# Kernel tuning notes

Hardware: AMD Instinct MI355X
Metric: run time of the kernel (lower is better)

## Reference

```python
import jax, jax.numpy as jnp
import numpy as np
from jax import lax

DIM = 2048
K = 3


def rms_norm(x):
    eps = jnp.asarray(jnp.finfo(x.dtype).eps, x.dtype)
    var = jnp.mean(jnp.square(x), axis=-1, keepdims=True)
    return x * lax.rsqrt(var + eps)


def causal_dwconv1d(y, w, b, dilation):
    # y: [B, S, D]; w: [D, 1, K]; depthwise causal conv along S
    yc = jnp.transpose(y, (0, 2, 1))  # [B, D, S]
    pad = (K - 1) * dilation
    out = lax.conv_general_dilated(
        yc, w.astype(yc.dtype),
        window_strides=(1,),
        padding=[(pad, 0)],
        rhs_dilation=(dilation,),
        dimension_numbers=('NCH', 'OIH', 'NCH'),
        feature_group_count=DIM,
    )
    out = out + b.astype(yc.dtype)[None, :, None]
    return jnp.transpose(out, (0, 2, 1))  # [B, S, D]


def setup_inputs() -> dict:
    key = jax.random.key(0)
    ks = jax.random.split(key, 4)
    B, S, D = 4, 4096, DIM
    x = jax.random.normal(ks[0], (B, S, D), dtype=jnp.float32)
    W_expand = jax.random.normal(ks[1], (3 * D, D), dtype=jnp.float32) * (1.0 / np.sqrt(D))
    conv_w = jax.random.normal(ks[2], (D, 1, K), dtype=jnp.float32) * (1.0 / K)
    conv_b = jnp.zeros((D,), dtype=jnp.float32)
    W_proj = jax.random.normal(ks[3], (D, D), dtype=jnp.float32) * (1.0 / np.sqrt(D))
    conv_scale = jnp.ones((D,), dtype=jnp.float32)
    return {"x": x, "W_expand": W_expand, "conv_w": conv_w, "conv_b": conv_b,
            "W_proj": W_proj, "conv_scale": conv_scale, "dilation": 1}


def reference(x, W_expand, conv_w, conv_b, W_proj, conv_scale, dilation):
    h = jnp.einsum('bsd,ed->bse', rms_norm(x), W_expand.astype(x.dtype))
    B_gate, C_gate, z = jnp.split(h, 3, axis=-1)
    y = B_gate * z  # squared_gate=False
    y = causal_dwconv1d(y, conv_w, conv_b, dilation)
    o = C_gate * y
    o = jnp.einsum('bsd,ed->bse', o, W_proj.astype(x.dtype))
    return x + conv_scale.astype(x.dtype)[None, None, :] * o
```

## Files before the change

kernel.cpp:

```cpp
#include <hip/hip_runtime.h>
#include <hip/hip_bf16.h>
#include <stdint.h>

typedef __bf16 bf16;
typedef __bf16 bf16x8 __attribute__((ext_vector_type(8)));
typedef __bf16 bf16x4 __attribute__((ext_vector_type(4)));
typedef float  floatx4 __attribute__((ext_vector_type(4)));

#define DIMD 2048
#define BATB 4
#define SEQS 4096
#define MTOT (BATB*SEQS)

#define BAR()    __builtin_amdgcn_s_barrier()
#define LGKMC(N) asm volatile("s_waitcnt lgkmcnt(" #N ")" ::: "memory")
#define VMC6()   asm volatile("s_waitcnt vmcnt(6)" ::: "memory")
#define VMC0()   asm volatile("s_waitcnt vmcnt(0)" ::: "memory")
#define SCHED0() __builtin_amdgcn_sched_barrier(0)

__device__ __forceinline__ void gload_lds16(const bf16* g, bf16* l) {
    __builtin_amdgcn_global_load_lds(
        (const __attribute__((address_space(1))) void*)g,
        (__attribute__((address_space(3))) void*)l,
        16, 0, 0);
}

__global__ __launch_bounds__(256) void f2bf_k(const float* __restrict__ src,
                                              bf16* __restrict__ dst, int n) {
    int i = (blockIdx.x * 256 + threadIdx.x) * 4;
    if (i >= n) return;
    float4 v = *(const float4*)&src[i];
    bf16x4 o;
    o[0] = (bf16)v.x; o[1] = (bf16)v.y; o[2] = (bf16)v.z; o[3] = (bf16)v.w;
    *(bf16x4*)&dst[i] = o;
}

__global__ __launch_bounds__(256) void rmsnorm_k(const float* __restrict__ x,
                                                 bf16* __restrict__ xn) {
    const int row = blockIdx.x;
    const int tid = threadIdx.x;
    const float* xr = x + (size_t)row * DIMD;
    float4 a = *(const float4*)&xr[tid * 8];
    float4 b = *(const float4*)&xr[tid * 8 + 4];
    float s = a.x*a.x + a.y*a.y + a.z*a.z + a.w*a.w
            + b.x*b.x + b.y*b.y + b.z*b.z + b.w*b.w;
    #pragma unroll
    for (int off = 32; off > 0; off >>= 1) s += __shfl_down(s, off);
    __shared__ float red[4];
    if ((tid & 63) == 0) red[tid >> 6] = s;
    __syncthreads();
    float tot = red[0] + red[1] + red[2] + red[3];
    float sc = rsqrtf(tot * (1.0f / DIMD) + 1.1920929e-07f);
    bf16x8 o;
    o[0] = (bf16)(a.x * sc); o[1] = (bf16)(a.y * sc);
    o[2] = (bf16)(a.z * sc); o[3] = (bf16)(a.w * sc);
    o[4] = (bf16)(b.x * sc); o[5] = (bf16)(b.y * sc);
    o[6] = (bf16)(b.z * sc); o[7] = (bf16)(b.w * sc);
    *(bf16x8*)&xn[(size_t)row * DIMD + tid * 8] = o;
}

__global__ __launch_bounds__(256) void gateconv_k(const bf16* __restrict__ h,
                                                  const float* __restrict__ cw,
                                                  const float* __restrict__ cb,
                                                  bf16* __restrict__ o,
                                                  const int* __restrict__ dil_p) {
    int gid = blockIdx.x * 256 + threadIdx.x;
    int m = gid >> 9;
    int d = (gid & 511) << 2;
    int s = m & (SEQS - 1);
    int dil = dil_p[0];
    const bf16* hr = h + (size_t)m * (3 * DIMD);

    bf16x4 Cv = *(const bf16x4*)&hr[DIMD + d];
    bf16x4 B0 = *(const bf16x4*)&hr[d];
    bf16x4 Z0 = *(const bf16x4*)&hr[2 * DIMD + d];
    float y0[4], y1[4], y2[4];
    #pragma unroll
    for (int j = 0; j < 4; ++j) y0[j] = (float)B0[j] * (float)Z0[j];
    if (s >= dil) {
        const bf16* h1 = hr - (size_t)dil * 3 * DIMD;
        bf16x4 B1 = *(const bf16x4*)&h1[d];
        bf16x4 Z1 = *(const bf16x4*)&h1[2 * DIMD + d];
        #pragma unroll
        for (int j = 0; j < 4; ++j) y1[j] = (float)B1[j] * (float)Z1[j];
    } else {
        #pragma unroll
        for (int j = 0; j < 4; ++j) y1[j] = 0.0f;
    }
    if (s >= 2 * dil) {
        const bf16* h2 = hr - (size_t)(2 * dil) * 3 * DIMD;
        bf16x4 B2 = *(const bf16x4*)&h2[d];
        bf16x4 Z2 = *(const bf16x4*)&h2[2 * DIMD + d];
        #pragma unroll
        for (int j = 0; j < 4; ++j) y2[j] = (float)B2[j] * (float)Z2[j];
    } else {
        #pragma unroll
        for (int j = 0; j < 4; ++j) y2[j] = 0.0f;
    }
    bf16x4 ov;
    #pragma unroll
    for (int j = 0; j < 4; ++j) {
        float w0 = cw[(d + j) * 3 + 0];
        float w1 = cw[(d + j) * 3 + 1];
        float w2 = cw[(d + j) * 3 + 2];
        float conv = w0 * y2[j] + w1 * y1[j] + w2 * y0[j] + cb[d + j];
        ov[j] = (bf16)((float)Cv[j] * conv);
    }
    *(bf16x4*)&o[(size_t)m * DIMD + d] = ov;
}

template<int RESID>
__global__ __launch_bounds__(512, 2) void gemm_bt(const bf16* __restrict__ A,
                                                  const bf16* __restrict__ B,
                                                  bf16* __restrict__ Hout,
                                                  float* __restrict__ Fout,
                                                  const float* __restrict__ resid,
                                                  const float* __restrict__ scale,
                                                  int M, int N, int K) {
    __shared__ __align__(16) bf16 smem[2][32768];
    const int tid = threadIdx.x;
    const int wave = tid >> 6;
    const int lane = tid & 63;
    const int quad = lane >> 4;
    const int col16 = lane & 15;

    const int nx   = (int)gridDim.x;
    const int nwg  = nx * (int)gridDim.y;
    const int orig = (int)blockIdx.y * nx + (int)blockIdx.x;
    const int lin  = (orig & 7) * (nwg >> 3) + (orig >> 3);
    const int n0 = (lin % nx) * 256;
    const int m0 = (lin / nx) * 256;

    const int wm = (wave >> 2) * 128;
    const int wn = (wave & 3) * 64;

    const int srow = tid >> 3;
    const int cs   = (tid & 7) ^ (srow & 7);
    const bf16* aSrc = A + (size_t)(m0 + srow) * K + cs * 8;
    const bf16* bSrc = B + (size_t)(n0 + srow) * K + cs * 8;
    const int stbase = wave * 512;
    const size_t K64  = (size_t)K * 64;
    const size_t K128 = (size_t)K * 128;

    const int rsw = col16 & 7;
    const int ard = (wm + col16) * 64;
    const int brd = (wn + col16) * 64;
    const int sl0 = ((0 + quad) ^ rsw) * 8;
    const int sl1 = ((4 + quad) ^ rsw) * 8;

    bf16x8 Bf[4][2];
    bf16x8 A0[2][2], A1[2][2], A2[2][2], A3[2][2];
    floatx4 acc[4][2][4];
    #pragma unroll
    for (int q = 0; q < 4; ++q)
        #pragma unroll
        for (int f = 0; f < 2; ++f)
            #pragma unroll
            for (int n = 0; n < 4; ++n) acc[q][f][n] = (floatx4)0.0f;

    auto stage = [&](const bf16* src, bf16* dstBase, int t, int h) {
        const bf16* s = src + (size_t)h * K128 + (size_t)t * 64;
        bf16* d = dstBase + h * 8192 + stbase;
        gload_lds16(s, d);
        gload_lds16(s + K64, d + 4096);
    };
    auto ldA = [&](bf16x8 (&q)[2][2], const bf16* Asb, int f0) {
        #pragma unroll
        for (int f = 0; f < 2; ++f) {
            const bf16* p = Asb + ard + (f0 + f) * (16 * 64);
            q[f][0] = *(const bf16x8*)(p + sl0);
            q[f][1] = *(const bf16x8*)(p + sl1);
        }
    };
    auto ldB = [&](const bf16* Bsb) {
        #pragma unroll
        for (int n = 0; n < 4; ++n) {
            const bf16* p = Bsb + brd + n * (16 * 64);
            Bf[n][0] = *(const bf16x8*)(p + sl0);
            Bf[n][1] = *(const bf16x8*)(p + sl1);
        }
    };
    auto mm = [&](floatx4 (&ac)[2][4], bf16x8 (&a)[2][2]) {
        __builtin_amdgcn_s_setprio(1);
        #pragma unroll
        for (int f = 0; f < 2; ++f)
            #pragma unroll
            for (int n = 0; n < 4; ++n) {
                ac[f][n] = __builtin_amdgcn_mfma_f32_16x16x32_bf16(a[f][0], Bf[n][0], ac[f][n], 0, 0, 0);
                ac[f][n] = __builtin_amdgcn_mfma_f32_16x16x32_bf16(a[f][1], Bf[n][1], ac[f][n], 0, 0, 0);
            }
        __builtin_amdgcn_s_setprio(0);
    };

    const int NT = K >> 6;

    stage(aSrc, smem[0],         0, 0);
    stage(aSrc, smem[0],         0, 1);
    stage(bSrc, smem[0] + 16384, 0, 0);
    stage(bSrc, smem[0] + 16384, 0, 1);
    stage(bSrc, smem[1] + 16384, 1, 0);
    stage(bSrc, smem[1] + 16384, 1, 1);
    stage(aSrc, smem[1],         1, 0);
    VMC6();
    BAR();
    ldB(smem[0] + 16384);
    ldA(A0, smem[0], 0);
    SCHED0();

    for (int t = 0; t < NT - 2; ++t) {
        const int b = t & 1;
        const bf16* Acur = smem[b];
        bf16* Awr = smem[b];
        bf16* Bwr = smem[b] + 16384;
        bf16* Aoth = smem[b ^ 1];
        const bf16* Anxt = smem[b ^ 1];
        const bf16* Bnxt = smem[b ^ 1] + 16384;
        ldA(A1, Acur, 2);
        stage(aSrc, Aoth, t + 1, 1);
        SCHED0(); BAR(); LGKMC(4); SCHED0();
        mm(acc[0], A0);
        BAR();
        ldA(A2, Acur, 4);
        stage(bSrc, Bwr, t + 2, 0);
        SCHED0(); BAR(); LGKMC(4); SCHED0();
        mm(acc[1], A1);
        BAR();
        ldA(A3, Acur, 6);
        stage(bSrc, Bwr, t + 2, 1);
        SCHED0(); BAR(); LGKMC(4); SCHED0();
        mm(acc[2], A2);
        BAR();
        stage(aSrc, Awr, t + 2, 0);
        VMC6();
        BAR(); LGKMC(0); SCHED0();
        mm(acc[3], A3);
        SCHED0();
        ldB(Bnxt);
        ldA(A0, Anxt, 0);
        SCHED0(); BAR();
    }
    {
        const int t = NT - 2;
        const int b = t & 1;
        const bf16* Acur = smem[b];
        bf16* Aoth = smem[b ^ 1];
        const bf16* Anxt = smem[b ^ 1];
        const bf16* Bnxt = smem[b ^ 1] + 16384;
        ldA(A1, Acur, 2);
        stage(aSrc, Aoth, t + 1, 1);
        SCHED0(); BAR(); LGKMC(4); SCHED0();
        mm(acc[0], A0);
        BAR();
        ldA(A2, Acur, 4);
        SCHED0(); BAR(); LGKMC(4); SCHED0();
        mm(acc[1], A1);
        BAR();
        ldA(A3, Acur, 6);
        SCHED0(); BAR(); LGKMC(4); SCHED0();
        mm(acc[2], A2);
        BAR();
        VMC0();
        BAR(); LGKMC(0); SCHED0();
        mm(acc[3], A3);
        SCHED0();
        ldB(Bnxt);
        ldA(A0, Anxt, 0);
        SCHED0(); BAR();
    }
    {
        const int b = (NT - 1) & 1;
        const bf16* Acur = smem[b];
        ldA(A1, Acur, 2);
        SCHED0(); BAR(); LGKMC(4); SCHED0();
        mm(acc[0], A0);
        BAR();
        ldA(A2, Acur, 4);
        SCHED0(); BAR(); LGKMC(4); SCHED0();
        mm(acc[1], A1);
        BAR();
        ldA(A3, Acur, 6);
        SCHED0(); BAR(); LGKMC(4); SCHED0();
        mm(acc[2], A2);
        BAR();
        LGKMC(0); SCHED0();
        mm(acc[3], A3);
    }

    #pragma unroll
    for (int q2 = 0; q2 < 4; ++q2)
        #pragma unroll
        for (int f = 0; f < 2; ++f)
            #pragma unroll
            for (int n = 0; n < 4; ++n) {
                const int c  = n0 + wn + n * 16 + col16;
                const int rb = m0 + wm + (q2 * 2 + f) * 16 + quad * 4;
                #pragma unroll
                for (int r = 0; r < 4; ++r) {
                    size_t off = (size_t)(rb + r) * N + c;
                    float v = acc[q2][f][n][r];
                    if (RESID) {
                        Fout[off] = resid[off] + scale[c] * v;
                    } else {
                        Hout[off] = (bf16)v;
                    }
                }
            }
}

extern "C" void kernel_launch(void* const* d_in, const int* in_sizes, int n_in,
                              void* d_out, int out_size, void* d_ws, size_t ws_size,
                              hipStream_t stream) {
    const float* x  = (const float*)d_in[0];
    const float* We = (const float*)d_in[1];
    const float* cw = (const float*)d_in[2];
    const float* cb = (const float*)d_in[3];
    const float* Wp = (const float*)d_in[4];
    const float* cs = (const float*)d_in[5];
    const int*   dil = (const int*)d_in[6];

    char* ws = (char*)d_ws;
    bf16* xn  = (bf16*)ws;
    bf16* Web = (bf16*)(ws + 67108864);
    bf16* Wpb = (bf16*)(ws + 67108864 + 25165824);
    bf16* h   = (bf16*)(ws + 100663296);

    f2bf_k<<<(3 * DIMD * DIMD / 4 + 255) / 256, 256, 0, stream>>>(We, Web, 3 * DIMD * DIMD);
    f2bf_k<<<(DIMD * DIMD / 4 + 255) / 256, 256, 0, stream>>>(Wp, Wpb, DIMD * DIMD);
    rmsnorm_k<<<MTOT, 256, 0, stream>>>(x, xn);
    gemm_bt<0><<<dim3(3 * DIMD / 256, MTOT / 256), 512, 0, stream>>>(
        xn, Web, h, nullptr, nullptr, nullptr, MTOT, 3 * DIMD, DIMD);
    gateconv_k<<<(MTOT * (DIMD / 4)) / 256, 256, 0, stream>>>(h, cw, cb, xn , dil);
    gemm_bt<1><<<dim3(DIMD / 256, MTOT / 256), 512, 0, stream>>>(
        xn , Wpb, nullptr, (float*)d_out, x, cs, MTOT, DIMD, DIMD);
}
```

Before: 836.9 us.

## Switch GEMM to 32x32x16 MFMA with coarser K-phase pipeline and nontemporal stores

```diff
diff --git a/kernel.cpp b/kernel.cpp
--- a/kernel.cpp
+++ b/kernel.cpp
@@ -5,7 +5,7 @@
 typedef __bf16 bf16;
 typedef __bf16 bf16x8 __attribute__((ext_vector_type(8)));
 typedef __bf16 bf16x4 __attribute__((ext_vector_type(4)));
-typedef float  floatx4 __attribute__((ext_vector_type(4)));
+typedef float  floatx16 __attribute__((ext_vector_type(16)));
 
 #define DIMD 2048
 #define BATB 4
@@ -14,7 +14,7 @@
 
 #define BAR()    __builtin_amdgcn_s_barrier()
 #define LGKMC(N) asm volatile("s_waitcnt lgkmcnt(" #N ")" ::: "memory")
-#define VMC6()   asm volatile("s_waitcnt vmcnt(6)" ::: "memory")
+#define VMC4()   asm volatile("s_waitcnt vmcnt(4)" ::: "memory")
 #define VMC0()   asm volatile("s_waitcnt vmcnt(0)" ::: "memory")
 #define SCHED0() __builtin_amdgcn_sched_barrier(0)
 
@@ -71,7 +71,7 @@
     int dil = dil_p[0];
     const bf16* hr = h + (size_t)m * (3 * DIMD);
 
-    bf16x4 Cv = *(const bf16x4*)&hr[DIMD + d];
+    bf16x4 Cv = __builtin_nontemporal_load((const bf16x4*)&hr[DIMD + d]);
     bf16x4 B0 = *(const bf16x4*)&hr[d];
     bf16x4 Z0 = *(const bf16x4*)&hr[2 * DIMD + d];
     float y0[4], y1[4], y2[4];
@@ -121,8 +121,9 @@
     const int tid = threadIdx.x;
     const int wave = tid >> 6;
     const int lane = tid & 63;
-    const int quad = lane >> 4;
-    const int col16 = lane & 15;
+    const int l31 = lane & 31;
+    const int hi = lane >> 5;
+    const int l7 = lane & 7;
 
     const int nx   = (int)gridDim.x;
     const int nwg  = nx * (int)gridDim.y;
@@ -142,21 +143,18 @@
     const size_t K64  = (size_t)K * 64;
     const size_t K128 = (size_t)K * 128;
 
-    const int rsw = col16 & 7;
-    const int ard = (wm + col16) * 64;
-    const int brd = (wn + col16) * 64;
-    const int sl0 = ((0 + quad) ^ rsw) * 8;
-    const int sl1 = ((4 + quad) ^ rsw) * 8;
-
-    bf16x8 Bf[4][2];
-    bf16x8 A0[2][2], A1[2][2], A2[2][2], A3[2][2];
-    floatx4 acc[4][2][4];
-    #pragma unroll
-    for (int q = 0; q < 4; ++q)
-        #pragma unroll
-        for (int f = 0; f < 2; ++f)
-            #pragma unroll
-            for (int n = 0; n < 4; ++n) acc[q][f][n] = (floatx4)0.0f;
+    const int arow = (wm + l31) * 64;
+    const int brow = (wn + l31) * 64;
+    const int slotk[4] = { ((0 + hi) ^ l7) * 8, ((2 + hi) ^ l7) * 8,
+                           ((4 + hi) ^ l7) * 8, ((6 + hi) ^ l7) * 8 };
+
+    bf16x8 Afr[4][4];
+    bf16x8 Bfr[4][2];
+    floatx16 acc[4][2];
+    #pragma unroll
+    for (int mi = 0; mi < 4; ++mi)
+        #pragma unroll
+        for (int ni = 0; ni < 2; ++ni) acc[mi][ni] = (floatx16)0.0f;
 
     auto stage = [&](const bf16* src, bf16* dstBase, int t, int h) {
         const bf16* s = src + (size_t)h * K128 + (size_t)t * 64;
@@ -164,32 +162,23 @@
         gload_lds16(s, d);
         gload_lds16(s + K64, d + 4096);
     };
-    auto ldA = [&](bf16x8 (&q)[2][2], const bf16* Asb, int f0) {
-        #pragma unroll
-        for (int f = 0; f < 2; ++f) {
-            const bf16* p = Asb + ard + (f0 + f) * (16 * 64);
-            q[f][0] = *(const bf16x8*)(p + sl0);
-            q[f][1] = *(const bf16x8*)(p + sl1);
-        }
+    auto ldAk = [&](const bf16* Asb, int ks) {
+        #pragma unroll
+        for (int mi = 0; mi < 4; ++mi)
+            Afr[ks][mi] = *(const bf16x8*)(Asb + arow + mi * (32 * 64) + slotk[ks]);
     };
-    auto ldB = [&](const bf16* Bsb) {
-        #pragma unroll
-        for (int n = 0; n < 4; ++n) {
-            const bf16* p = Bsb + brd + n * (16 * 64);
-            Bf[n][0] = *(const bf16x8*)(p + sl0);
-            Bf[n][1] = *(const bf16x8*)(p + sl1);
-        }
+    auto ldBk = [&](const bf16* Bsb, int ks) {
+        #pragma unroll
+        for (int ni = 0; ni < 2; ++ni)
+            Bfr[ks][ni] = *(const bf16x8*)(Bsb + brow + ni * (32 * 64) + slotk[ks]);
     };
-    auto mm = [&](floatx4 (&ac)[2][4], bf16x8 (&a)[2][2]) {
-        __builtin_amdgcn_s_setprio(1);
-        #pragma unroll
-        for (int f = 0; f < 2; ++f)
+    auto mmk = [&](int ks) {
+        #pragma unroll
+        for (int mi = 0; mi < 4; ++mi)
             #pragma unroll
-            for (int n = 0; n < 4; ++n) {
-                ac[f][n] = __builtin_amdgcn_mfma_f32_16x16x32_bf16(a[f][0], Bf[n][0], ac[f][n], 0, 0, 0);
-                ac[f][n] = __builtin_amdgcn_mfma_f32_16x16x32_bf16(a[f][1], Bf[n][1], ac[f][n], 0, 0, 0);
-            }
-        __builtin_amdgcn_s_setprio(0);
+            for (int ni = 0; ni < 2; ++ni)
+                acc[mi][ni] = __builtin_amdgcn_mfma_f32_32x32x16_bf16(
+                    Afr[ks][mi], Bfr[ks][ni], acc[mi][ni], 0, 0, 0);
     };
 
     const int NT = K >> 6;
@@ -200,43 +189,38 @@
     stage(bSrc, smem[0] + 16384, 0, 1);
     stage(bSrc, smem[1] + 16384, 1, 0);
     stage(bSrc, smem[1] + 16384, 1, 1);
-    stage(aSrc, smem[1],         1, 0);
-    VMC6();
+    VMC4();
     BAR();
-    ldB(smem[0] + 16384);
-    ldA(A0, smem[0], 0);
+    ldBk(smem[0] + 16384, 0); ldBk(smem[0] + 16384, 1);
+    ldBk(smem[0] + 16384, 2); ldBk(smem[0] + 16384, 3);
+    ldAk(smem[0], 0); ldAk(smem[0], 1);
     SCHED0();
 
     for (int t = 0; t < NT - 2; ++t) {
         const int b = t & 1;
         const bf16* Acur = smem[b];
-        bf16* Awr = smem[b];
         bf16* Bwr = smem[b] + 16384;
         bf16* Aoth = smem[b ^ 1];
         const bf16* Anxt = smem[b ^ 1];
         const bf16* Bnxt = smem[b ^ 1] + 16384;
-        ldA(A1, Acur, 2);
+        ldAk(Acur, 2); ldAk(Acur, 3);
+        stage(aSrc, Aoth, t + 1, 0);
         stage(aSrc, Aoth, t + 1, 1);
-        SCHED0(); BAR(); LGKMC(4); SCHED0();
-        mm(acc[0], A0);
+        SCHED0(); BAR(); LGKMC(8); SCHED0();
+        __builtin_amdgcn_s_setprio(1);
+        mmk(0); mmk(1);
+        __builtin_amdgcn_s_setprio(0);
         BAR();
-        ldA(A2, Acur, 4);
         stage(bSrc, Bwr, t + 2, 0);
-        SCHED0(); BAR(); LGKMC(4); SCHED0();
-        mm(acc[1], A1);
-        BAR();
-        ldA(A3, Acur, 6);
         stage(bSrc, Bwr, t + 2, 1);
-        SCHED0(); BAR(); LGKMC(4); SCHED0();
-        mm(acc[2], A2);
-        BAR();
-        stage(aSrc, Awr, t + 2, 0);
-        VMC6();
+        VMC4();
         BAR(); LGKMC(0); SCHED0();
-        mm(acc[3], A3);
+        __builtin_amdgcn_s_setprio(1);
+        mmk(2); mmk(3);
+        __builtin_amdgcn_s_setprio(0);
         SCHED0();
-        ldB(Bnxt);
-        ldA(A0, Anxt, 0);
+        ldBk(Bnxt, 0); ldBk(Bnxt, 1); ldBk(Bnxt, 2); ldBk(Bnxt, 3);
+        ldAk(Anxt, 0); ldAk(Anxt, 1);
         SCHED0(); BAR();
     }
     {
@@ -246,65 +230,57 @@
         bf16* Aoth = smem[b ^ 1];
         const bf16* Anxt = smem[b ^ 1];
         const bf16* Bnxt = smem[b ^ 1] + 16384;
-        ldA(A1, Acur, 2);
+        ldAk(Acur, 2); ldAk(Acur, 3);
+        stage(aSrc, Aoth, t + 1, 0);
         stage(aSrc, Aoth, t + 1, 1);
-        SCHED0(); BAR(); LGKMC(4); SCHED0();
-        mm(acc[0], A0);
-        BAR();
-        ldA(A2, Acur, 4);
-        SCHED0(); BAR(); LGKMC(4); SCHED0();
-        mm(acc[1], A1);
-        BAR();
-        ldA(A3, Acur, 6);
-        SCHED0(); BAR(); LGKMC(4); SCHED0();
-        mm(acc[2], A2);
+        SCHED0(); BAR(); LGKMC(8); SCHED0();
+        __builtin_amdgcn_s_setprio(1);
+        mmk(0); mmk(1);
+        __builtin_amdgcn_s_setprio(0);
         BAR();
         VMC0();
         BAR(); LGKMC(0); SCHED0();
-        mm(acc[3], A3);
+        __builtin_amdgcn_s_setprio(1);
+        mmk(2); mmk(3);
+        __builtin_amdgcn_s_setprio(0);
         SCHED0();
-        ldB(Bnxt);
-        ldA(A0, Anxt, 0);
+        ldBk(Bnxt, 0); ldBk(Bnxt, 1); ldBk(Bnxt, 2); ldBk(Bnxt, 3);
+        ldAk(Anxt, 0); ldAk(Anxt, 1);
         SCHED0(); BAR();
     }
     {
         const int b = (NT - 1) & 1;
         const bf16* Acur = smem[b];
-        ldA(A1, Acur, 2);
-        SCHED0(); BAR(); LGKMC(4); SCHED0();
-        mm(acc[0], A0);
-        BAR();
-        ldA(A2, Acur, 4);
-        SCHED0(); BAR(); LGKMC(4); SCHED0();
-        mm(acc[1], A1);
-        BAR();
-        ldA(A3, Acur, 6);
-        SCHED0(); BAR(); LGKMC(4); SCHED0();
-        mm(acc[2], A2);
-        BAR();
+        ldAk(Acur, 2); ldAk(Acur, 3);
+        SCHED0(); BAR(); LGKMC(8); SCHED0();
+        __builtin_amdgcn_s_setprio(1);
+        mmk(0); mmk(1);
+        __builtin_amdgcn_s_setprio(0);
         LGKMC(0); SCHED0();
-        mm(acc[3], A3);
-    }
-
-    #pragma unroll
-    for (int q2 = 0; q2 < 4; ++q2)
-        #pragma unroll
-        for (int f = 0; f < 2; ++f)
+        __builtin_amdgcn_s_setprio(1);
+        mmk(2); mmk(3);
+        __builtin_amdgcn_s_setprio(0);
+    }
+
+    #pragma unroll
+    for (int mi = 0; mi < 4; ++mi)
+        #pragma unroll
+        for (int ni = 0; ni < 2; ++ni) {
+            const int c  = n0 + wn + ni * 32 + l31;
+            const int rb = m0 + wm + mi * 32 + 4 * hi;
             #pragma unroll
-            for (int n = 0; n < 4; ++n) {
-                const int c  = n0 + wn + n * 16 + col16;
-                const int rb = m0 + wm + (q2 * 2 + f) * 16 + quad * 4;
-                #pragma unroll
-                for (int r = 0; r < 4; ++r) {
-                    size_t off = (size_t)(rb + r) * N + c;
-                    float v = acc[q2][f][n][r];
-                    if (RESID) {
-                        Fout[off] = resid[off] + scale[c] * v;
-                    } else {
-                        Hout[off] = (bf16)v;
-                    }
+            for (int reg = 0; reg < 16; ++reg) {
+                const int r = rb + (reg & 3) + 8 * (reg >> 2);
+                size_t off = (size_t)r * N + c;
+                float v = acc[mi][ni][reg];
+                if (RESID) {
+                    float rv = __builtin_nontemporal_load(&resid[off]);
+                    __builtin_nontemporal_store(rv + scale[c] * v, &Fout[off]);
+                } else {
+                    __builtin_nontemporal_store((bf16)v, &Hout[off]);
                 }
             }
+        }
 }
 
 extern "C" void kernel_launch(void* const* d_in, const int* in_sizes, int n_in,
```

Result: slower. 878.5 us (+5.0%).

## Tile gateconv over 16 sequence rows with a register sliding window

Applied to the files above, without the earlier changes.

```diff
diff --git a/kernel.cpp b/kernel.cpp
--- a/kernel.cpp
+++ b/kernel.cpp
@@ -64,49 +64,95 @@
                                                   const float* __restrict__ cb,
                                                   bf16* __restrict__ o,
                                                   const int* __restrict__ dil_p) {
-    int gid = blockIdx.x * 256 + threadIdx.x;
-    int m = gid >> 9;
-    int d = (gid & 511) << 2;
-    int s = m & (SEQS - 1);
-    int dil = dil_p[0];
-    const bf16* hr = h + (size_t)m * (3 * DIMD);
-
-    bf16x4 Cv = *(const bf16x4*)&hr[DIMD + d];
-    bf16x4 B0 = *(const bf16x4*)&hr[d];
-    bf16x4 Z0 = *(const bf16x4*)&hr[2 * DIMD + d];
-    float y0[4], y1[4], y2[4];
+    const int tid = threadIdx.x;
+    const int d = tid * 8;
+    const int m0 = blockIdx.x * 16;
+    const int s0 = m0 & (SEQS - 1);
+    const int dil = dil_p[0];
+
+    float w0[8], w1[8], w2[8], bias[8];
     #pragma unroll
-    for (int j = 0; j < 4; ++j) y0[j] = (float)B0[j] * (float)Z0[j];
-    if (s >= dil) {
-        const bf16* h1 = hr - (size_t)dil * 3 * DIMD;
-        bf16x4 B1 = *(const bf16x4*)&h1[d];
-        bf16x4 Z1 = *(const bf16x4*)&h1[2 * DIMD + d];
-        #pragma unroll
-        for (int j = 0; j < 4; ++j) y1[j] = (float)B1[j] * (float)Z1[j];
+    for (int j = 0; j < 8; ++j) {
+        w0[j]   = cw[(d + j) * 3 + 0];
+        w1[j]   = cw[(d + j) * 3 + 1];
+        w2[j]   = cw[(d + j) * 3 + 2];
+        bias[j] = cb[d + j];
+    }
+
+    if (dil == 1) {
+        float y1[8], y2[8];
+        if (s0 >= 1) {
+            const bf16* hp = h + (size_t)(m0 - 1) * (3 * DIMD);
+            bf16x8 Bv = *(const bf16x8*)&hp[d];
+            bf16x8 Zv = *(const bf16x8*)&hp[2 * DIMD + d];
+            #pragma unroll
+            for (int j = 0; j < 8; ++j) y1[j] = (float)Bv[j] * (float)Zv[j];
+            const bf16* hq = h + (size_t)(m0 - 2) * (3 * DIMD);
+            bf16x8 Bw = *(const bf16x8*)&hq[d];
+            bf16x8 Zw = *(const bf16x8*)&hq[2 * DIMD + d];
+            #pragma unroll
+            for (int j = 0; j < 8; ++j) y2[j] = (float)Bw[j] * (float)Zw[j];
+        } else {
+            #pragma unroll
+            for (int j = 0; j < 8; ++j) { y1[j] = 0.0f; y2[j] = 0.0f; }
+        }
+        for (int r = 0; r < 16; ++r) {
+            const bf16* hr = h + (size_t)(m0 + r) * (3 * DIMD);
+            bf16x8 Bv = *(const bf16x8*)&hr[d];
+            bf16x8 Zv = *(const bf16x8*)&hr[2 * DIMD + d];
+            bf16x8 Cv = *(const bf16x8*)&hr[DIMD + d];
+            float y0[8];
+            bf16x8 ov;
+            #pragma unroll
+            for (int j = 0; j < 8; ++j) {
+                y0[j] = (float)Bv[j] * (float)Zv[j];
+                float conv = w0[j] * y2[j] + w1[j] * y1[j] + w2[j] * y0[j] + bias[j];
+                ov[j] = (bf16)((float)Cv[j] * conv);
+            }
+            *(bf16x8*)&o[(size_t)(m0 + r) * DIMD + d] = ov;
+            #pragma unroll
+            for (int j = 0; j < 8; ++j) { y2[j] = y1[j]; y1[j] = y0[j]; }
+        }
     } else {
-        #pragma unroll
-        for (int j = 0; j < 4; ++j) y1[j] = 0.0f;
-    }
-    if (s >= 2 * dil) {
-        const bf16* h2 = hr - (size_t)(2 * dil) * 3 * DIMD;
-        bf16x4 B2 = *(const bf16x4*)&h2[d];
-        bf16x4 Z2 = *(const bf16x4*)&h2[2 * DIMD + d];
-        #pragma unroll
-        for (int j = 0; j < 4; ++j) y2[j] = (float)B2[j] * (float)Z2[j];
-    } else {
-        #pragma unroll
-        for (int j = 0; j < 4; ++j) y2[j] = 0.0f;
-    }
-    bf16x4 ov;
-    #pragma unroll
-    for (int j = 0; j < 4; ++j) {
-        float w0 = cw[(d + j) * 3 + 0];
-        float w1 = cw[(d + j) * 3 + 1];
-        float w2 = cw[(d + j) * 3 + 2];
-        float conv = w0 * y2[j] + w1 * y1[j] + w2 * y0[j] + cb[d + j];
-        ov[j] = (bf16)((float)Cv[j] * conv);
-    }
-    *(bf16x4*)&o[(size_t)m * DIMD + d] = ov;
+        for (int r = 0; r < 16; ++r) {
+            const int m = m0 + r;
+            const int s = m & (SEQS - 1);
+            const bf16* hr = h + (size_t)m * (3 * DIMD);
+            bf16x8 Bv = *(const bf16x8*)&hr[d];
+            bf16x8 Zv = *(const bf16x8*)&hr[2 * DIMD + d];
+            bf16x8 Cv = *(const bf16x8*)&hr[DIMD + d];
+            float y0[8], y1[8], y2[8];
+            #pragma unroll
+            for (int j = 0; j < 8; ++j) y0[j] = (float)Bv[j] * (float)Zv[j];
+            if (s >= dil) {
+                const bf16* h1 = hr - (size_t)dil * 3 * DIMD;
+                bf16x8 B1 = *(const bf16x8*)&h1[d];
+                bf16x8 Z1 = *(const bf16x8*)&h1[2 * DIMD + d];
+                #pragma unroll
+                for (int j = 0; j < 8; ++j) y1[j] = (float)B1[j] * (float)Z1[j];
+            } else {
+                #pragma unroll
+                for (int j = 0; j < 8; ++j) y1[j] = 0.0f;
+            }
+            if (s >= 2 * dil) {
+                const bf16* h2 = hr - (size_t)(2 * dil) * 3 * DIMD;
+                bf16x8 B2 = *(const bf16x8*)&h2[d];
+                bf16x8 Z2 = *(const bf16x8*)&h2[2 * DIMD + d];
+                #pragma unroll
+                for (int j = 0; j < 8; ++j) y2[j] = (float)B2[j] * (float)Z2[j];
+            } else {
+                #pragma unroll
+                for (int j = 0; j < 8; ++j) y2[j] = 0.0f;
+            }
+            bf16x8 ov;
+            #pragma unroll
+            for (int j = 0; j < 8; ++j) {
+                float conv = w0[j] * y2[j] + w1[j] * y1[j] + w2[j] * y0[j] + bias[j];
+                ov[j] = (bf16)((float)Cv[j] * conv);
+            }
+            *(bf16x8*)&o[(size_t)m * DIMD + d] = ov;
+        }
+    }
 }
 
 template<int RESID>
@@ -329,7 +375,7 @@
     rmsnorm_k<<<MTOT, 256, 0, stream>>>(x, xn);
     gemm_bt<0><<<dim3(3 * DIMD / 256, MTOT / 256), 512, 0, stream>>>(
         xn, Web, h, nullptr, nullptr, nullptr, MTOT, 3 * DIMD, DIMD);
-    gateconv_k<<<(MTOT * (DIMD / 4)) / 256, 256, 0, stream>>>(h, cw, cb, xn , dil);
+    gateconv_k<<<MTOT / 16, 256, 0, stream>>>(h, cw, cb, xn , dil);
     gemm_bt<1><<<dim3(DIMD / 256, MTOT / 256), 512, 0, stream>>>(
         xn , Wpb, nullptr, (float*)d_out, x, cs, MTOT, DIMD, DIMD);
 }
```

After: 825.7 us. About the same (-1.3%).
